# Performance work log

Measured on AMD Instinct MI355X. Metric: run time of the kernel, lower is better.

## Reference

```python
import jax, jax.numpy as jnp
import numpy as np

DIM_IN = 512
DIM_OUT = 64


def setup_inputs() -> dict:
    key = jax.random.key(0)
    kx, kq, kk, kv = jax.random.split(key, 4)
    x = jax.random.normal(kx, (4, 4096, DIM_IN), dtype=jnp.float32)
    s = 1.0 / np.sqrt(DIM_IN)
    # torch nn.Linear stores weight as [out, in]; keep same convention
    Wq = jax.random.uniform(kq, (DIM_OUT, DIM_IN), jnp.float32, -s, s)
    Wk = jax.random.uniform(kk, (DIM_OUT, DIM_IN), jnp.float32, -s, s)
    Wv = jax.random.uniform(kv, (DIM_OUT, DIM_IN), jnp.float32, -s, s)
    return {"x": x, "Wq": Wq, "Wk": Wk, "Wv": Wv}


def reference(x, Wq, Wk, Wv):
    # q/k/v projections: [B,S,Din] @ [Din,Dout] -> [B,S,Dout]
    q = jnp.einsum("bsd,od->bso", x, Wq)
    k = jnp.einsum("bsd,od->bso", x, Wk)
    v = jnp.einsum("bsd,od->bso", x, Wv)
    scale = 1.0 / jnp.sqrt(jnp.asarray(q.shape[-1], q.dtype))
    scores = jnp.einsum("bqo,bko->bqk", q, k) * scale  # [B,S,S]
    weights = jax.nn.softmax(scores, axis=-1)
    out = jnp.einsum("bqk,bko->bqo", weights, v)  # [B,S,Dout]
    return out
```

## Files before the change

### kernel.cpp

```cpp
#include <hip/hip_runtime.h>
#include <hip/hip_bf16.h>

#define SEQ 4096
#define MTOT 16384

typedef float f32x4  __attribute__((ext_vector_type(4)));
typedef float f32x16 __attribute__((ext_vector_type(16)));
typedef _Float16 f16;
typedef _Float16 f16x4 __attribute__((ext_vector_type(4)));
typedef _Float16 f16x8 __attribute__((ext_vector_type(8)));
typedef unsigned int   u32;
typedef unsigned int   u32x2 __attribute__((ext_vector_type(2)));
typedef unsigned short u16;

static constexpr size_t QL_B   = 0;
static constexpr size_t KL_B   = 2u << 20;
static constexpr size_t VL_B   = 4u << 20;
static constexpr size_t WL_B   = 6u << 20;
static constexpr size_t PART_B = 8u << 20;
static constexpr size_t ML_B   = 42u << 20;

__device__ __forceinline__ u16 h16(float v) { return __builtin_bit_cast(u16, (f16)v); }
__device__ __forceinline__ u32 pkrtz(float a, float b) {
  return __builtin_bit_cast(u32, __builtin_amdgcn_cvt_pkrtz(a, b));
}
__device__ __forceinline__ void gl16(const u16* g, u16* l) {
  __builtin_amdgcn_global_load_lds((const __attribute__((address_space(1))) void*)g,
                                   (__attribute__((address_space(3))) void*)l, 16, 0, 0);
}

__global__ __launch_bounds__(256) void wconv_kernel(const float* __restrict__ Wq,
                                                    const float* __restrict__ Wk,
                                                    const float* __restrict__ Wv,
                                                    u16* __restrict__ wlin) {
  const float QSC = 0.18033688011112042f;
  int e = blockIdx.x * 256 + threadIdx.x;
  int flat = e * 4;
  int colg = flat >> 9;
  int k0   = flat & 511;
  int mat  = colg >> 6;
  const float* W = (mat == 0) ? Wq : (mat == 1 ? Wk : Wv);
  f32x4 v = *(const f32x4*)(W + (size_t)(colg & 63) * 512 + k0);
  if (mat == 0) v *= QSC;
  int s = colg >> 4, r16 = colg & 15;
  int step = k0 >> 5, g = (k0 & 31) >> 3, jb = k0 & 7;
  __attribute__((aligned(8))) u16 b[4];
#pragma unroll
  for (int j = 0; j < 4; ++j) b[j] = h16(v[j]);
  *(uint2*)(wlin + ((size_t)(s * 16 + step) * 64 + g * 16 + r16) * 8 + jb) = *(uint2*)b;
}

__global__ __launch_bounds__(256, 4) void proj_kernel(const float* __restrict__ x,
                                                      const u16* __restrict__ wlin,
                                                      u16* __restrict__ ws) {
  __shared__ __attribute__((aligned(16))) u16 xl[8192];
  float* scr = (float*)xl;

  const int tid  = threadIdx.x;
  const int blk  = blockIdx.x;
  const int lane = tid & 63;
  const int ng   = tid >> 6;
  const int r16  = lane & 15;
  const int g    = lane >> 4;
  const int m0   = blk * 16;

#pragma unroll
  for (int i = 0; i < 8; ++i) {
    int f = tid * 4 + i * 1024;
    int row = f >> 9, k0 = f & 511;
    f32x4 v = *(const f32x4*)(x + (size_t)m0 * 512 + f);
    __attribute__((aligned(8))) u16 b[4];
#pragma unroll
    for (int j = 0; j < 4; ++j) b[j] = h16(v[j]);
    int ln = ((k0 & 31) >> 3) * 16 + row;
    *(uint2*)(xl + ((size_t)(k0 >> 5) * 64 + ln) * 8 + (k0 & 7)) = *(uint2*)b;
  }
  __syncthreads();

  f32x4 acc[3];
#pragma unroll
  for (int s = 0; s < 3; ++s) acc[s] = (f32x4){0.f, 0.f, 0.f, 0.f};

#pragma unroll 2
  for (int step = 0; step < 16; ++step) {
    f16x8 a = *(const f16x8*)(xl + ((size_t)step * 64 + lane) * 8);
#pragma unroll
    for (int s = 0; s < 3; ++s) {
      int sg = ng * 3 + s;
      f16x8 b = *(const f16x8*)(wlin + ((size_t)(sg * 16 + step) * 64 + lane) * 8);
      acc[s] = __builtin_amdgcn_mfma_f32_16x16x32_f16(a, b, acc[s], 0, 0, 0);
    }
  }
  __syncthreads();

#pragma unroll
  for (int s = 0; s < 3; ++s)
#pragma unroll
    for (int rr = 0; rr < 4; ++rr)
      scr[(g * 4 + rr) * 193 + ng * 48 + s * 16 + r16] = acc[s][rr];
  __syncthreads();

  u16* Ql = ws + (QL_B >> 1);
  u16* Kl = ws + (KL_B >> 1);
  u16* Vl = ws + (VL_B >> 1);
  const int batch = m0 >> 12;
  const int tile  = (m0 >> 5) & 127;
  const int half  = (m0 >> 4) & 1;

  {
    int t2 = tid & 127;
    int r  = t2 & 15, hh = (t2 >> 4) & 1, ch = t2 >> 5;
    int l31 = half * 16 + r;
    __attribute__((aligned(16))) u16 b[8];
    if (tid < 128) {
#pragma unroll
      for (int j = 0; j < 8; ++j) b[j] = h16(scr[r * 193 + 64 + ch * 16 + hh * 8 + j]);
      *(uint4*)(Kl + ((size_t)((batch * 128 + tile) * 4 + ch) * 64 + hh * 32 + l31) * 8) =
          *(uint4*)b;
    } else {
#pragma unroll
      for (int j = 0; j < 8; ++j) b[j] = h16(scr[r * 193 + ch * 16 + hh * 8 + j]);
      int qhalf = (m0 >> 5);
      *(uint4*)(Ql + ((size_t)(qhalf * 4 + ch) * 64 + hh * 32 + l31) * 8) = *(uint4*)b;
    }
  }
  {
    int z = tid & 1, l31 = (tid >> 1) & 31, hh = (tid >> 6) & 1, db = tid >> 7;
    int d = db * 32 + l31;
    __attribute__((aligned(8))) u16 b[4];
#pragma unroll
    for (int j = 0; j < 4; ++j) b[j] = h16(scr[(8 * z + 4 * hh + j) * 193 + 128 + d]);
    *(uint2*)(Vl + ((size_t)(((batch * 128 + tile) * 2 + db) * 2 + half) * 64 + hh * 32 + l31) *
                       8 + z * 4) = *(uint2*)b;
  }
}

__global__ __launch_bounds__(1024, 4) void attn_kernel(u16* __restrict__ ws) {
  __shared__ __attribute__((aligned(16))) u16 kvbuf[2][2][2048];

  const int tid  = threadIdx.x;
  const int w    = tid >> 6;
  const int lane = tid & 63;
  const int l31  = lane & 31;
  const int h    = lane >> 5;
  const int bx   = blockIdx.x;
  const int qb   = bx >> 3;
  const int sp   = bx & 7;
  const int bb   = qb >> 3;
  const int q0   = qb * 512 + w * 32;

  const u16* Ql = ws + (QL_B >> 1);
  const u16* Kl = ws + (KL_B >> 1);
  const u16* Vl = ws + (VL_B >> 1);

  const int qhalf = qb * 16 + w;
  f16x8 qf[4];
#pragma unroll
  for (int ch = 0; ch < 4; ++ch)
    qf[ch] = *(const f16x8*)(Ql + ((size_t)(qhalf * 4 + ch) * 64 + lane) * 8);

  f32x16 oacc[2];
#pragma unroll
  for (int db = 0; db < 2; ++db)
#pragma unroll
    for (int r = 0; r < 16; ++r) oacc[db][r] = 0.f;
  float mrun = -INFINITY, lrun = 0.f;
  const float RTHR = 11.0f;

  const int kt0 = bb * 128 + sp * 16;

  if (w == 15) {
    const u16* ks = Kl + (size_t)kt0 * 2048;
    const u16* vs = Vl + (size_t)kt0 * 2048;
#pragma unroll
    for (int c = 0; c < 4; ++c) gl16(ks + c * 512 + lane * 8, &kvbuf[0][0][c * 512]);
#pragma unroll
    for (int c = 0; c < 4; ++c) gl16(vs + c * 512 + lane * 8, &kvbuf[0][1][c * 512]);
  }
  __syncthreads();

#pragma unroll 1
  for (int it = 0; it < 16; ++it) {
    const int cur = it & 1;
    if (w == 15 && it < 15) {
      const u16* ks = Kl + (size_t)(kt0 + it + 1) * 2048;
      const u16* vs = Vl + (size_t)(kt0 + it + 1) * 2048;
#pragma unroll
      for (int c = 0; c < 4; ++c) gl16(ks + c * 512 + lane * 8, &kvbuf[cur ^ 1][0][c * 512]);
#pragma unroll
      for (int c = 0; c < 4; ++c) gl16(vs + c * 512 + lane * 8, &kvbuf[cur ^ 1][1][c * 512]);
    }

    f16x8 ka[4], vp[2][2];
#pragma unroll
    for (int ch = 0; ch < 4; ++ch)
      ka[ch] = *(const f16x8*)&kvbuf[cur][0][(ch * 64 + lane) * 8];
#pragma unroll
    for (int db = 0; db < 2; ++db)
#pragma unroll
      for (int p = 0; p < 2; ++p)
        vp[db][p] = *(const f16x8*)&kvbuf[cur][1][((db * 2 + p) * 64 + lane) * 8];

    f32x16 sac;
#pragma unroll
    for (int r = 0; r < 16; ++r) sac[r] = 0.f;
#pragma unroll
    for (int ch = 0; ch < 4; ++ch)
      sac = __builtin_amdgcn_mfma_f32_32x32x16_f16(ka[ch], qf[ch], sac, 0, 0, 0);

    float mt = sac[0];
#pragma unroll
    for (int r = 1; r < 16; ++r) mt = fmaxf(mt, sac[r]);
    if (__any(mt > mrun + RTHR)) {
      float mtw  = fmaxf(mt, __shfl_xor(mt, 32));
      float nm   = fmaxf(mrun, mtw);
      float corr = exp2f(mrun - nm);
      lrun *= corr;
      mrun = nm;
#pragma unroll
      for (int db = 0; db < 2; ++db)
#pragma unroll
        for (int r = 0; r < 16; ++r) oacc[db][r] *= corr;
    }
#pragma unroll
    for (int r = 0; r < 16; ++r) {
      float pv = exp2f(sac[r] - mrun);
      sac[r] = pv;
      lrun += pv;
    }

    f16x4 pb[4];
#pragma unroll
    for (int c = 0; c < 4; ++c) {
      u32x2 pk;
      pk[0] = pkrtz(sac[4 * c + 0], sac[4 * c + 1]);
      pk[1] = pkrtz(sac[4 * c + 2], sac[4 * c + 3]);
      pb[c] = __builtin_bit_cast(f16x4, pk);
    }

#pragma unroll
    for (int db = 0; db < 2; ++db)
#pragma unroll
      for (int p = 0; p < 2; ++p) {
        f16x4 vlo = __builtin_shufflevector(vp[db][p], vp[db][p], 0, 1, 2, 3);
        f16x4 vhi = __builtin_shufflevector(vp[db][p], vp[db][p], 4, 5, 6, 7);
        oacc[db] = __builtin_amdgcn_mfma_f32_32x32x8f16(vlo, pb[2 * p], oacc[db], 0, 0, 0);
        oacc[db] = __builtin_amdgcn_mfma_f32_32x32x8f16(vhi, pb[2 * p + 1], oacc[db], 0, 0, 0);
      }

    __syncthreads();
  }

  lrun += __shfl_xor(lrun, 32);

  float* Op = (float*)((char*)ws + PART_B) + (size_t)sp * MTOT * 64;
#pragma unroll
  for (int db = 0; db < 2; ++db)
#pragma unroll
    for (int r = 0; r < 16; ++r) {
      int d = db * 32 + (r & 3) + 8 * (r >> 2) + 4 * h;
      Op[(size_t)(q0 + l31) * 64 + d] = oacc[db][r];
    }
  if (h == 0) {
    float* Mm = (float*)((char*)ws + ML_B);
    float* Ll = Mm + 8 * MTOT;
    Mm[(size_t)sp * MTOT + q0 + l31] = mrun;
    Ll[(size_t)sp * MTOT + q0 + l31] = lrun;
  }
}

__global__ __launch_bounds__(256) void merge_kernel(const u16* __restrict__ ws,
                                                    float* __restrict__ out) {
  int gid = blockIdx.x * 256 + threadIdx.x;
  int row = gid >> 2, dg = gid & 3;
  const float* Mm = (const float*)((const char*)ws + ML_B);
  const float* Ll = Mm + 8 * MTOT;
  float mv[8];
  float mg = -INFINITY;
#pragma unroll
  for (int i = 0; i < 8; ++i) {
    mv[i] = Mm[(size_t)i * MTOT + row];
    mg = fmaxf(mg, mv[i]);
  }
  float den = 0.f, wv[8];
#pragma unroll
  for (int i = 0; i < 8; ++i) {
    wv[i] = exp2f(mv[i] - mg);
    den += wv[i] * Ll[(size_t)i * MTOT + row];
  }
  f32x4 acc[4];
#pragma unroll
  for (int m = 0; m < 4; ++m) acc[m] = (f32x4){0.f, 0.f, 0.f, 0.f};
  const float* Op = (const float*)((const char*)ws + PART_B);
#pragma unroll
  for (int i = 0; i < 8; ++i)
#pragma unroll
    for (int m = 0; m < 4; ++m) {
      f32x4 t = *(const f32x4*)(Op + ((size_t)i * MTOT + row) * 64 + dg * 16 + m * 4);
      acc[m] += wv[i] * t;
    }
  float inv = 1.f / den;
#pragma unroll
  for (int m = 0; m < 4; ++m) {
    f32x4 r = acc[m] * inv;
    *(f32x4*)(out + (size_t)row * 64 + dg * 16 + m * 4) = r;
  }
}

extern "C" void kernel_launch(void* const* d_in, const int* in_sizes, int n_in,
                              void* d_out, int out_size, void* d_ws, size_t ws_size,
                              hipStream_t stream) {
  const float* x  = (const float*)d_in[0];
  const float* Wq = (const float*)d_in[1];
  const float* Wk = (const float*)d_in[2];
  const float* Wv = (const float*)d_in[3];
  u16* ws = (u16*)d_ws;
  (void)in_sizes; (void)n_in; (void)out_size; (void)ws_size;

  wconv_kernel<<<96, 256, 0, stream>>>(Wq, Wk, Wv, ws + (WL_B >> 1));
  proj_kernel<<<1024, 256, 0, stream>>>(x, ws + (WL_B >> 1), ws);
  attn_kernel<<<256, 1024, 0, stream>>>(ws);
  merge_kernel<<<256, 256, 0, stream>>>(ws, (float*)d_out);
}
```

Baseline: 65.81 us.

## Halve attention block size, stage two KV tiles per barrier across all waves

```diff
diff --git a/kernel.cpp b/kernel.cpp
--- a/kernel.cpp
+++ b/kernel.cpp
@@ -135,8 +135,8 @@
   }
 }
 
-__global__ __launch_bounds__(1024, 4) void attn_kernel(u16* __restrict__ ws) {
-  __shared__ __attribute__((aligned(16))) u16 kvbuf[2][2][2048];
+__global__ __launch_bounds__(512, 4) void attn_kernel(u16* __restrict__ ws) {
+  __shared__ __attribute__((aligned(16))) u16 kvb[2][8192];
 
   const int tid  = threadIdx.x;
   const int w    = tid >> 6;
@@ -146,14 +146,14 @@
   const int bx   = blockIdx.x;
   const int qb   = bx >> 3;
   const int sp   = bx & 7;
-  const int bb   = qb >> 3;
-  const int q0   = qb * 512 + w * 32;
+  const int bb   = qb >> 4;
+  const int q0   = qb * 256 + w * 32;
 
   const u16* Ql = ws + (QL_B >> 1);
   const u16* Kl = ws + (KL_B >> 1);
   const u16* Vl = ws + (VL_B >> 1);
 
-  const int qhalf = qb * 16 + w;
+  const int qhalf = qb * 8 + w;
   f16x8 qf[4];
 #pragma unroll
   for (int ch = 0; ch < 4; ++ch)
@@ -169,85 +169,88 @@
 
   const int kt0 = bb * 128 + sp * 16;
 
-  if (w == 15) {
-    const u16* ks = Kl + (size_t)kt0 * 2048;
-    const u16* vs = Vl + (size_t)kt0 * 2048;
-#pragma unroll
-    for (int c = 0; c < 4; ++c) gl16(ks + c * 512 + lane * 8, &kvbuf[0][0][c * 512]);
-#pragma unroll
-    for (int c = 0; c < 4; ++c) gl16(vs + c * 512 + lane * 8, &kvbuf[0][1][c * 512]);
-  }
+  auto stage = [&](int b, int p) {
+#pragma unroll
+    for (int cc = 0; cc < 2; ++cc) {
+      const int c = w * 2 + cc;
+      const u16* src;
+      if (c < 8) {
+        src = Kl + (size_t)(kt0 + p * 2 + (c >> 2)) * 2048 + (c & 3) * 512 + lane * 8;
+      } else {
+        const int c2 = c - 8;
+        src = Vl + (size_t)(kt0 + p * 2 + (c2 >> 2)) * 2048 + (c2 & 3) * 512 + lane * 8;
+      }
+      gl16(src, &kvb[b][c * 512]);
+    }
+  };
+
+  stage(0, 0);
   __syncthreads();
 
 #pragma unroll 1
-  for (int it = 0; it < 16; ++it) {
-    const int cur = it & 1;
-    if (w == 15 && it < 15) {
-      const u16* ks = Kl + (size_t)(kt0 + it + 1) * 2048;
-      const u16* vs = Vl + (size_t)(kt0 + it + 1) * 2048;
-#pragma unroll
-      for (int c = 0; c < 4; ++c) gl16(ks + c * 512 + lane * 8, &kvbuf[cur ^ 1][0][c * 512]);
-#pragma unroll
-      for (int c = 0; c < 4; ++c) gl16(vs + c * 512 + lane * 8, &kvbuf[cur ^ 1][1][c * 512]);
-    }
-
-    f16x8 ka[4], vp[2][2];
-#pragma unroll
-    for (int ch = 0; ch < 4; ++ch)
-      ka[ch] = *(const f16x8*)&kvbuf[cur][0][(ch * 64 + lane) * 8];
-#pragma unroll
-    for (int db = 0; db < 2; ++db)
-#pragma unroll
-      for (int p = 0; p < 2; ++p)
-        vp[db][p] = *(const f16x8*)&kvbuf[cur][1][((db * 2 + p) * 64 + lane) * 8];
-
-    f32x16 sac;
-#pragma unroll
-    for (int r = 0; r < 16; ++r) sac[r] = 0.f;
-#pragma unroll
-    for (int ch = 0; ch < 4; ++ch)
-      sac = __builtin_amdgcn_mfma_f32_32x32x16_f16(ka[ch], qf[ch], sac, 0, 0, 0);
-
-    float mt = sac[0];
-#pragma unroll
-    for (int r = 1; r < 16; ++r) mt = fmaxf(mt, sac[r]);
-    if (__any(mt > mrun + RTHR)) {
-      float mtw  = fmaxf(mt, __shfl_xor(mt, 32));
-      float nm   = fmaxf(mrun, mtw);
-      float corr = exp2f(mrun - nm);
-      lrun *= corr;
-      mrun = nm;
+  for (int p = 0; p < 8; ++p) {
+    const int cur = p & 1;
+    if (p < 7) stage(cur ^ 1, p + 1);
+
+#pragma unroll
+    for (int s = 0; s < 2; ++s) {
+      f16x8 ka[4], vp[2][2];
+#pragma unroll
+      for (int ch = 0; ch < 4; ++ch)
+        ka[ch] = *(const f16x8*)&kvb[cur][((s << 2) + ch) * 512 + lane * 8];
 #pragma unroll
       for (int db = 0; db < 2; ++db)
 #pragma unroll
-        for (int r = 0; r < 16; ++r) oacc[db][r] *= corr;
-    }
-#pragma unroll
-    for (int r = 0; r < 16; ++r) {
-      float pv = exp2f(sac[r] - mrun);
-      sac[r] = pv;
-      lrun += pv;
-    }
-
-    f16x4 pb[4];
-#pragma unroll
-    for (int c = 0; c < 4; ++c) {
-      u32x2 pk;
-      pk[0] = pkrtz(sac[4 * c + 0], sac[4 * c + 1]);
-      pk[1] = pkrtz(sac[4 * c + 2], sac[4 * c + 3]);
-      pb[c] = __builtin_bit_cast(f16x4, pk);
-    }
-
-#pragma unroll
-    for (int db = 0; db < 2; ++db)
-#pragma unroll
-      for (int p = 0; p < 2; ++p) {
-        f16x4 vlo = __builtin_shufflevector(vp[db][p], vp[db][p], 0, 1, 2, 3);
-        f16x4 vhi = __builtin_shufflevector(vp[db][p], vp[db][p], 4, 5, 6, 7);
-        oacc[db] = __builtin_amdgcn_mfma_f32_32x32x8f16(vlo, pb[2 * p], oacc[db], 0, 0, 0);
-        oacc[db] = __builtin_amdgcn_mfma_f32_32x32x8f16(vhi, pb[2 * p + 1], oacc[db], 0, 0, 0);
+        for (int pp = 0; pp < 2; ++pp)
+          vp[db][pp] = *(const f16x8*)&kvb[cur][(8 + (s << 2) + db * 2 + pp) * 512 + lane * 8];
+
+      f32x16 sac;
+#pragma unroll
+      for (int r = 0; r < 16; ++r) sac[r] = 0.f;
+#pragma unroll
+      for (int ch = 0; ch < 4; ++ch)
+        sac = __builtin_amdgcn_mfma_f32_32x32x16_f16(ka[ch], qf[ch], sac, 0, 0, 0);
+
+      float mt = sac[0];
+#pragma unroll
+      for (int r = 1; r < 16; ++r) mt = fmaxf(mt, sac[r]);
+      if (__any(mt > mrun + RTHR)) {
+        float mtw  = fmaxf(mt, __shfl_xor(mt, 32));
+        float nm   = fmaxf(mrun, mtw);
+        float corr = exp2f(mrun - nm);
+        lrun *= corr;
+        mrun = nm;
+#pragma unroll
+        for (int db = 0; db < 2; ++db)
+#pragma unroll
+          for (int r = 0; r < 16; ++r) oacc[db][r] *= corr;
       }
-
+#pragma unroll
+      for (int r = 0; r < 16; ++r) {
+        float pv = exp2f(sac[r] - mrun);
+        sac[r] = pv;
+        lrun += pv;
+      }
+
+      f16x4 pb[4];
+#pragma unroll
+      for (int c = 0; c < 4; ++c) {
+        u32x2 pk;
+        pk[0] = pkrtz(sac[4 * c + 0], sac[4 * c + 1]);
+        pk[1] = pkrtz(sac[4 * c + 2], sac[4 * c + 3]);
+        pb[c] = __builtin_bit_cast(f16x4, pk);
+      }
+
+#pragma unroll
+      for (int db = 0; db < 2; ++db)
+#pragma unroll
+        for (int pp = 0; pp < 2; ++pp) {
+          f16x4 vlo = __builtin_shufflevector(vp[db][pp], vp[db][pp], 0, 1, 2, 3);
+          f16x4 vhi = __builtin_shufflevector(vp[db][pp], vp[db][pp], 4, 5, 6, 7);
+          oacc[db] = __builtin_amdgcn_mfma_f32_32x32x8f16(vlo, pb[2 * pp], oacc[db], 0, 0, 0);
+          oacc[db] = __builtin_amdgcn_mfma_f32_32x32x8f16(vhi, pb[2 * pp + 1], oacc[db], 0, 0, 0);
+        }
+    }
     __syncthreads();
   }
 
@@ -319,6 +322,6 @@
 
   wconv_kernel<<<96, 256, 0, stream>>>(Wq, Wk, Wv, ws + (WL_B >> 1));
   proj_kernel<<<1024, 256, 0, stream>>>(x, ws + (WL_B >> 1), ws);
-  attn_kernel<<<256, 1024, 0, stream>>>(ws);
+  attn_kernel<<<512, 512, 0, stream>>>(ws);
   merge_kernel<<<256, 256, 0, stream>>>(ws, (float*)d_out);
 }
```

Result: no change. 64.69 us (-1.7%).
